# Kernel optimization log

Hardware: AMD Instinct MI355X
Metric: run time of the kernel (lower is better)

Reference implementation:

```python
import jax, jax.numpy as jnp
import numpy as np

N_NODES = 100000
N_EDGES = 1600000
N_FEAT = 128
HIDDEN = 128
N_CLASSES = 10
N_GRAPHS = 64


def setup_inputs() -> dict:
    key = jax.random.key(0)
    ks = jax.random.split(key, 9)
    x = jax.random.normal(ks[0], (N_NODES, N_FEAT), dtype=jnp.float32)
    edge_index = jax.random.randint(ks[1], (2, N_EDGES), 0, N_NODES, dtype=jnp.int64)
    batch = jnp.sort(jax.random.randint(ks[2], (N_NODES,), 0, N_GRAPHS, dtype=jnp.int64))
    # GCNConv weights (stored as [in, out] for x @ W) and biases
    s1 = 1.0 / np.sqrt(N_FEAT)
    s2 = 1.0 / np.sqrt(HIDDEN)
    W1 = jax.random.uniform(ks[3], (N_FEAT, HIDDEN), jnp.float32, -s1, s1)
    b1 = jnp.zeros((HIDDEN,), jnp.float32)
    W2 = jax.random.uniform(ks[4], (HIDDEN, HIDDEN), jnp.float32, -s2, s2)
    b2 = jnp.zeros((HIDDEN,), jnp.float32)
    Wfc = jax.random.uniform(ks[5], (HIDDEN, N_CLASSES), jnp.float32, -s2, s2)
    bfc = jax.random.uniform(ks[6], (N_CLASSES,), jnp.float32, -s2, s2)
    return {"x": x, "edge_index": edge_index, "batch": batch,
            "W1": W1, "b1": b1, "W2": W2, "b2": b2, "Wfc": Wfc, "bfc": bfc}


def gcn_conv(x, W, b, src, dst, n_nodes):
    # PyG GCNConv: add self-loops, symmetric normalization D^-1/2 A D^-1/2,
    # linear transform, scatter-add aggregation, plus bias.
    h = x @ W  # [N, H]
    deg = jax.ops.segment_sum(jnp.ones_like(dst, dtype=x.dtype), dst,
                              num_segments=n_nodes)  # in-degree incl. self loops
    dis = jnp.where(deg > 0, jax.lax.rsqrt(deg), 0.0)
    norm = dis[src] * dis[dst]  # [E+N]
    msg = h[src] * norm[:, None]  # gather + scale
    out = jax.ops.segment_sum(msg, dst, num_segments=n_nodes)  # scatter-add
    return out + b


def reference(x, edge_index, batch, W1, b1, W2, b2, Wfc, bfc):
    n = x.shape[0]
    loops = jnp.arange(n, dtype=edge_index.dtype)
    src = jnp.concatenate([edge_index[0], loops])
    dst = jnp.concatenate([edge_index[1], loops])

    h = jax.nn.relu(gcn_conv(x, W1, b1, src, dst, n))
    h = jax.nn.relu(gcn_conv(h, W2, b2, src, dst, n))

    # global_mean_pool over graph ids
    sums = jax.ops.segment_sum(h, batch, num_segments=N_GRAPHS)  # [B, H]
    cnts = jax.ops.segment_sum(jnp.ones((n,), h.dtype), batch,
                               num_segments=N_GRAPHS)
    pooled = sums / jnp.maximum(cnts, 1.0)[:, None]
    return pooled @ Wfc + bfc  # [B, C]
```

## Files before the change

kernel.cpp:

```cpp
#include <hip/hip_runtime.h>
#include <hip/hip_bf16.h>


typedef __attribute__((ext_vector_type(8))) short s16x8;
typedef __attribute__((ext_vector_type(4))) float f32x4;

#define BSH 9
#define BNODES 512
#define SRC_BITS 17
#define SRC_MASK ((1u << SRC_BITS) - 1u)
#define EPB 4096
#define NPART 8
#define PSH 14

__device__ inline float bflo(unsigned int u) { return __uint_as_float(u << 16); }
__device__ inline float bfhi(unsigned int u) { return __uint_as_float(u & 0xFFFF0000u); }
__device__ inline unsigned short f2bf(float f) {
    unsigned int u = __float_as_uint(f);
    unsigned int r = (u + 0x7FFFu + ((u >> 16) & 1u)) >> 16;
    return (unsigned short)r;
}
__device__ inline unsigned int packbf2(float a, float b) {
    return (unsigned int)f2bf(a) | ((unsigned int)f2bf(b) << 16);
}

__global__ __launch_bounds__(512) void bucket_scatter_kernel(const int* __restrict__ src, const int* __restrict__ dst,
                                                             int E, int cap, int* __restrict__ gfill,
                                                             unsigned int* __restrict__ gbuf, int nsc,
                                                             const float* __restrict__ W1, const float* __restrict__ W2,
                                                             short* __restrict__ WT1, short* __restrict__ WT2,
                                                             short* __restrict__ bufA, int n) {
    __shared__ int hist[256];
    __shared__ int loff[256];
    __shared__ int basea[256];
    __shared__ int rk[256];
    __shared__ int wsum[4];
    __shared__ unsigned int sorted[EPB];
    __shared__ unsigned char bko[EPB];
    int t = threadIdx.x;
    if ((int)blockIdx.x >= nsc) {
        int g = ((int)blockIdx.x - nsc) * 512 + t;
        const float* W = (g < 16384) ? W1 : W2;
        short* WT = (g < 16384) ? WT1 : WT2;
        int tt = g & 16383;
        int k = tt >> 7, nn = tt & 127;
        WT[nn * 128 + k] = f2bf(W[tt]);
        if ((int)blockIdx.x == nsc && t < 64) ((unsigned int*)(bufA + (size_t)n * 128))[t] = 0u;
        return;
    }
    if (t < 256) { hist[t] = 0; rk[t] = 0; }
    __syncthreads();
    int e0 = blockIdx.x * EPB;
    unsigned int wreg[EPB / 512];
    int breg[EPB / 512];
    #pragma unroll
    for (int i = 0; i < EPB / 512; i++) {
        int e = e0 + i * 512 + t;
        if (e < E) {
            int d = dst[e], s = src[e];
            int b = d >> BSH;
            wreg[i] = ((unsigned int)(d & (BNODES - 1)) << SRC_BITS) | (unsigned int)s;
            breg[i] = b;
            atomicAdd(&hist[b], 1);
        } else breg[i] = -1;
    }
    __syncthreads();
    int h = 0, incl = 0;
    if (t < 256) {
        h = hist[t];
        incl = h;
        int lane = t & 63;
        #pragma unroll
        for (int d = 1; d < 64; d <<= 1) {
            int u = __shfl_up(incl, d);
            if (lane >= d) incl += u;
        }
        if (lane == 63) wsum[t >> 6] = incl;
    }
    __syncthreads();
    if (t < 256) {
        int w = t >> 6;
        int wbase = 0;
        #pragma unroll
        for (int i = 0; i < 4; i++) if (i < w) wbase += wsum[i];
        loff[t] = wbase + incl - h;
        basea[t] = (h > 0) ? atomicAdd(&gfill[t], h) : 0;
    }
    __syncthreads();
    #pragma unroll
    for (int i = 0; i < EPB / 512; i++) {
        int b = breg[i];
        if (b >= 0) {
            int slot = loff[b] + atomicAdd(&rk[b], 1);
            sorted[slot] = wreg[i];
            bko[slot] = (unsigned char)b;
        }
    }
    __syncthreads();
    int ntot = loff[255] + hist[255];
    for (int i = t; i < ntot; i += 512) {
        int b = bko[i];
        int pos = basea[b] + (i - loff[b]);
        if (pos < cap) gbuf[(size_t)b * cap + pos] = sorted[i];
    }
}

__global__ __launch_bounds__(1024) void bucket_countfill_kernel(const unsigned int* __restrict__ gbuf,
                                                                const int* __restrict__ gfill, int cap, int n,
                                                                int* __restrict__ cnt, int* __restrict__ offA,
                                                                float* __restrict__ dis, int* __restrict__ g_total,
                                                                int* __restrict__ csr) {
    int b = blockIdx.x, t = threadIdx.x;
    int d0 = b << BSH;
    __shared__ int cl2[BNODES * NPART];
    __shared__ int nodeoff[BNODES];
    __shared__ int wsum[4];
    __shared__ int gbase_s;
    for (int i = t; i < BNODES * NPART; i += 1024) cl2[i] = 0;
    __syncthreads();
    int ne = min(gfill[b], cap);
    const unsigned int* eb = gbuf + (size_t)b * cap;
    for (int i = t; i < ne; i += 1024) {
        unsigned int wd = eb[i];
        int li = wd >> SRC_BITS;
        int part = (int)((wd & SRC_MASK) >> PSH);
        atomicAdd(&cl2[li * NPART + part], 1);
    }
    __syncthreads();
    int v0 = 0, v1 = 0, p0 = 0, p1 = 0, incl = 0, s = 0;
    if (t < 256) {
        #pragma unroll
        for (int j = 0; j < NPART; j++) v0 += cl2[(2 * t) * NPART + j];
        #pragma unroll
        for (int j = 0; j < NPART; j++) v1 += cl2[(2 * t + 1) * NPART + j];
        p0 = (v0 + 7) & ~7; p1 = (v1 + 7) & ~7;
        s = p0 + p1;
        incl = s;
        int lane = t & 63;
        #pragma unroll
        for (int dd = 1; dd < 64; dd <<= 1) {
            int u = __shfl_up(incl, dd);
            if (lane >= dd) incl += u;
        }
        if (lane == 63) wsum[t >> 6] = incl;
    }
    __syncthreads();
    if (t == 0) gbase_s = atomicAdd(g_total, wsum[0] + wsum[1] + wsum[2] + wsum[3]);
    __syncthreads();
    if (t < 256) {
        int w = t >> 6;
        int wbase = 0;
        #pragma unroll
        for (int i = 0; i < 4; i++) if (i < w) wbase += wsum[i];
        int excl = wbase + incl - s;
        int gbase = gbase_s;
        int o0 = gbase + excl, o1 = o0 + p0;
        int i0 = d0 + 2 * t, i1 = i0 + 1;
        if (i0 < n) { cnt[i0] = p0; offA[i0] = o0; dis[i0] = rsqrtf((float)(v0 + 1)); }
        if (i1 < n) { cnt[i1] = p1; offA[i1] = o1; dis[i1] = rsqrtf((float)(v1 + 1)); }
        nodeoff[2 * t] = o0; nodeoff[2 * t + 1] = o1;
    }
    __syncthreads();
    if (t < BNODES) {
        int run = nodeoff[t];
        #pragma unroll
        for (int j = 0; j < NPART; j++) {
            int c = cl2[t * NPART + j];
            cl2[t * NPART + j] = run;
            run += c;
        }
    }
    __syncthreads();
    for (int i = t; i < ne; i += 1024) {
        unsigned int wd = eb[i];
        int li = wd >> SRC_BITS;
        int part = (int)((wd & SRC_MASK) >> PSH);
        int slot = atomicAdd(&cl2[li * NPART + part], 1);
        csr[slot] = (int)(wd & SRC_MASK);
    }
    __syncthreads();
    if (t < BNODES) {
        int base = nodeoff[t];
        int end = cl2[t * NPART + NPART - 1];
        int p = ((end - base) + 7) & ~7;
        for (int j = end; j < base + p; j++) csr[j] = n;
    }
}

template <bool F32IN>
__global__ __launch_bounds__(256) void gemm_mfma_kernel(const void* __restrict__ Xv, const short* __restrict__ WTb,
                                                        const float* __restrict__ dis,
                                                        short* __restrict__ Yb, int n, int ntiles) {
    int lane = threadIdx.x & 63;
    int m = lane & 15, kg = lane >> 4;
    int gwave = (int)((blockIdx.x * 256 + threadIdx.x) >> 6);
    if (gwave >= ntiles) return;

    s16x8 bfr[8][4];
    #pragma unroll
    for (int t = 0; t < 8; t++)
        #pragma unroll
        for (int ks = 0; ks < 4; ks++)
            bfr[t][ks] = *(const s16x8*)(WTb + ((m * 8 + t) * 128 + ks * 32 + kg * 8));

    int rbase = gwave * 16;
    int row = rbase + m;
    size_t rc = (size_t)(row < n ? row : n - 1);
    s16x8 afr[4];
    if constexpr (F32IN) {
        const float* xrow = (const float*)Xv + rc * 128 + kg * 8;
        #pragma unroll
        for (int ks = 0; ks < 4; ks++) {
            float4 a0 = *(const float4*)(xrow + ks * 32);
            float4 a1 = *(const float4*)(xrow + ks * 32 + 4);
            s16x8 f;
            f[0] = (short)f2bf(a0.x); f[1] = (short)f2bf(a0.y);
            f[2] = (short)f2bf(a0.z); f[3] = (short)f2bf(a0.w);
            f[4] = (short)f2bf(a1.x); f[5] = (short)f2bf(a1.y);
            f[6] = (short)f2bf(a1.z); f[7] = (short)f2bf(a1.w);
            afr[ks] = f;
        }
    } else {
        const short* xrow = (const short*)Xv + rc * 128 + kg * 8;
        #pragma unroll
        for (int ks = 0; ks < 4; ks++) afr[ks] = *(const s16x8*)(xrow + ks * 32);
    }
    f32x4 acc[8];
    #pragma unroll
    for (int t = 0; t < 8; t++) acc[t] = (f32x4)(0.f);
    #pragma unroll
    for (int ks = 0; ks < 4; ks++)
        #pragma unroll
        for (int t = 0; t < 8; t++)
            acc[t] = __builtin_amdgcn_mfma_f32_16x16x32_bf16(afr[ks], bfr[t][ks], acc[t], 0, 0, 0);
    int orow0 = rbase + kg * 4;
    #pragma unroll
    for (int r = 0; r < 4; r++) {
        int orow = orow0 + r;
        if (orow < n) {
            float dv = dis[orow];
            s16x8 y;
            #pragma unroll
            for (int t = 0; t < 8; t++) y[t] = (short)f2bf(acc[t][r] * dv);
            *(s16x8*)(Yb + (size_t)orow * 128 + m * 8) = y;
        }
    }
}

__global__ __launch_bounds__(256) void agg_kernel(const short* __restrict__ H, const int* __restrict__ csr,
                                                  const int* __restrict__ offA, const int* __restrict__ cnt,
                                                  const float* __restrict__ dis, const float* __restrict__ bias,
                                                  short* __restrict__ O, int n) {
    int wid = __builtin_amdgcn_readfirstlane((int)((blockIdx.x * 256 + threadIdx.x) >> 6));
    int lane = threadIdx.x & 63;
    int half = lane >> 5, fl = lane & 31;
    if (wid >= n) return;
    int base = __builtin_amdgcn_readfirstlane(offA[wid]);
    int c = __builtin_amdgcn_readfirstlane(cnt[wid]);
    float d = dis[wid];
    float a0 = 0.f, a1 = 0.f, a2 = 0.f, a3 = 0.f;
    if (half == 0) {
        uint2 sv = ((const uint2*)(H + (size_t)wid * 128))[fl];
        a0 = bflo(sv.x); a1 = bfhi(sv.x);
        a2 = bflo(sv.y); a3 = bfhi(sv.y);
    }
    for (int k = 0; k < c; k += 8) {
        int4 q0 = *(const int4*)(csr + base + k);
        int4 q1 = *(const int4*)(csr + base + k + 4);
        int r0 = half ? q0.y : q0.x;
        int r1 = half ? q0.w : q0.z;
        int r2 = half ? q1.y : q1.x;
        int r3 = half ? q1.w : q1.z;
        uint2 h0 = ((const uint2*)(H + (size_t)r0 * 128))[fl];
        uint2 h1 = ((const uint2*)(H + (size_t)r1 * 128))[fl];
        uint2 h2 = ((const uint2*)(H + (size_t)r2 * 128))[fl];
        uint2 h3 = ((const uint2*)(H + (size_t)r3 * 128))[fl];
        a0 += bflo(h0.x); a1 += bfhi(h0.x); a2 += bflo(h0.y); a3 += bfhi(h0.y);
        a0 += bflo(h1.x); a1 += bfhi(h1.x); a2 += bflo(h1.y); a3 += bfhi(h1.y);
        a0 += bflo(h2.x); a1 += bfhi(h2.x); a2 += bflo(h2.y); a3 += bfhi(h2.y);
        a0 += bflo(h3.x); a1 += bfhi(h3.x); a2 += bflo(h3.y); a3 += bfhi(h3.y);
    }
    a0 += __shfl_xor(a0, 32);
    a1 += __shfl_xor(a1, 32);
    a2 += __shfl_xor(a2, 32);
    a3 += __shfl_xor(a3, 32);
    if (half == 0) {
        float4 b = ((const float4*)bias)[fl];
        float o0 = a0 * d + b.x, o1 = a1 * d + b.y;
        float o2 = a2 * d + b.z, o3 = a3 * d + b.w;
        o0 = fmaxf(o0, 0.f); o1 = fmaxf(o1, 0.f);
        o2 = fmaxf(o2, 0.f); o3 = fmaxf(o3, 0.f);
        ((uint2*)(O + (size_t)wid * 128))[fl] = make_uint2(packbf2(o0, o1), packbf2(o2, o3));
    }
}

__global__ __launch_bounds__(1024) void poolfc_kernel(const short* __restrict__ H, const int* __restrict__ batch,
                                                      const float* __restrict__ Wfc, const float* __restrict__ bfc,
                                                      float* __restrict__ out, int n) {
    int g = blockIdx.x;
    int t = threadIdx.x;
    int w = t >> 6, lane = t & 63;
    int q = lane >> 4, fl4 = lane & 15;
    int lo = 0, hi = n;
    while (lo < hi) { int mid = (lo + hi) >> 1; if (batch[mid] < g) lo = mid + 1; else hi = mid; }
    int lo2 = lo; hi = n;
    while (lo2 < hi) { int mid = (lo2 + hi) >> 1; if (batch[mid] < g + 1) lo2 = mid + 1; else hi = mid; }
    float ac[8];
    #pragma unroll
    for (int j = 0; j < 8; j++) ac[j] = 0.f;
    for (int i = lo + w * 4 + q; i < lo2; i += 64) {
        uint4 u = ((const uint4*)(H + (size_t)i * 128))[fl4];
        ac[0] += bflo(u.x); ac[1] += bfhi(u.x);
        ac[2] += bflo(u.y); ac[3] += bfhi(u.y);
        ac[4] += bflo(u.z); ac[5] += bfhi(u.z);
        ac[6] += bflo(u.w); ac[7] += bfhi(u.w);
    }
    #pragma unroll
    for (int j = 0; j < 8; j++) {
        ac[j] += __shfl_xor(ac[j], 16);
        ac[j] += __shfl_xor(ac[j], 32);
    }
    __shared__ float red[16][128];
    if (lane < 16) {
        #pragma unroll
        for (int j = 0; j < 8; j++) red[w][fl4 * 8 + j] = ac[j];
    }
    __syncthreads();
    __shared__ float pv[128];
    if (w == 0) {
        float s0 = 0.f, s1 = 0.f;
        #pragma unroll
        for (int r = 0; r < 16; r++) { s0 += red[r][2 * lane]; s1 += red[r][2 * lane + 1]; }
        float inv = 1.0f / fmaxf((float)(lo2 - lo), 1.0f);
        pv[2 * lane] = s0 * inv;
        pv[2 * lane + 1] = s1 * inv;
    }
    __syncthreads();
    if (t < 10) {
        float acc = 0.f;
        for (int k = 0; k < 128; k++) acc += pv[k] * Wfc[k * 10 + t];
        out[g * 10 + t] = acc + bfc[t];
    }
}

extern "C" void kernel_launch(void* const* d_in, const int* in_sizes, int n_in,
                              void* d_out, int out_size, void* d_ws, size_t ws_size,
                              hipStream_t stream) {
    const float* x   = (const float*)d_in[0];
    const int*   ei  = (const int*)d_in[1];
    const int*   bat = (const int*)d_in[2];
    const float* W1  = (const float*)d_in[3];
    const float* b1  = (const float*)d_in[4];
    const float* W2  = (const float*)d_in[5];
    const float* b2  = (const float*)d_in[6];
    const float* Wfc = (const float*)d_in[7];
    const float* bfc = (const float*)d_in[8];
    int n = in_sizes[0] / 128;
    int E = in_sizes[1] / 2;
    const int* src = ei;
    const int* dst = ei + E;

    int nbuck = (n + BNODES - 1) >> BSH;
    int cap = ((E / nbuck) * 2 + 512 + 63) & ~63;

    char* ws = (char*)d_ws;
    size_t off = 0;
    auto alloc = [&](size_t bytes) -> void* {
        void* p = ws + off;
        off = (off + bytes + 511) & ~(size_t)511;
        return p;
    };
    int*   gfill  = (int*)alloc(256 * 4);
    int*   gtotal = (int*)alloc(512);
    size_t zero_bytes = off;
    int*   cnt   = (int*)alloc((size_t)n * 4);
    int*   offA  = (int*)alloc((size_t)n * 4);
    float* dis   = (float*)alloc((size_t)n * 4);
    unsigned int* gbuf = (unsigned int*)alloc((size_t)nbuck * cap * 4);
    int*   csr   = (int*)alloc(((size_t)E + 8 * (size_t)(n + 1)) * 4);
    short* wt1   = (short*)alloc(128 * 128 * 2);
    short* wt2   = (short*)alloc(128 * 128 * 2);
    short* bufA  = (short*)alloc((size_t)(n + 1) * 128 * 2);
    short* bufB  = (short*)alloc((size_t)(n + 1) * 128 * 2);
    (void)ws_size;

    int ntiles = (n + 15) / 16;
    int gemm_blocks = (ntiles + 3) / 4;
    int nsc = (E + EPB - 1) / EPB;

    hipMemsetAsync(d_ws, 0, zero_bytes, stream);
    bucket_scatter_kernel<<<nsc + 64, 512, 0, stream>>>(src, dst, E, cap, gfill, gbuf, nsc,
                                                        W1, W2, wt1, wt2, bufA, n);
    bucket_countfill_kernel<<<nbuck, 1024, 0, stream>>>(gbuf, gfill, cap, n, cnt, offA, dis, gtotal, csr);

    gemm_mfma_kernel<true><<<gemm_blocks, 256, 0, stream>>>(x, wt1, dis, bufA, n, ntiles);
    agg_kernel<<<((size_t)n * 64 + 255) / 256, 256, 0, stream>>>(bufA, csr, offA, cnt, dis, b1, bufB, n);
    gemm_mfma_kernel<false><<<gemm_blocks, 256, 0, stream>>>(bufB, wt2, dis, bufA, n, ntiles);
    agg_kernel<<<((size_t)n * 64 + 255) / 256, 256, 0, stream>>>(bufA, csr, offA, cnt, dis, b2, bufB, n);

    poolfc_kernel<<<64, 1024, 0, stream>>>(bufB, bat, Wfc, bfc, (float*)d_out, n);
}
```

Measured before the change: 332.8 us.

## Fuse CSR build with first GEMM, stage weights in LDS, split pooling

Buckets now hold 256 nodes and the CSR build drops its per-source partitioning, so rows are padded to 4 instead of 8. The first-layer GEMM runs in the same launch as the CSR build, as extra blocks that no longer need dis, so it can proceed without waiting for degrees. The source-side normalization moves into the first aggregation, which now gathers dis per neighbour. Both GEMMs stage the transposed weights in LDS across 1024-thread blocks instead of loading them into registers per wave. Pooling is split into a 256-block partial-sum kernel and a small FC kernel to raise parallelism. The cost is extra gathers of dis in layer-1 aggregation, plus a changed sort locality that drops the source partitioning.

```diff
diff --git a/kernel.cpp b/kernel.cpp
--- a/kernel.cpp
+++ b/kernel.cpp
@@ -5,13 +5,11 @@
 typedef __attribute__((ext_vector_type(8))) short s16x8;
 typedef __attribute__((ext_vector_type(4))) float f32x4;
 
-#define BSH 9
-#define BNODES 512
+#define BSH 8
+#define BNODES 256
 #define SRC_BITS 17
 #define SRC_MASK ((1u << SRC_BITS) - 1u)
 #define EPB 4096
-#define NPART 8
-#define PSH 14
 
 __device__ inline float bflo(unsigned int u) { return __uint_as_float(u << 16); }
 __device__ inline float bfhi(unsigned int u) { return __uint_as_float(u & 0xFFFF0000u); }
@@ -30,13 +28,13 @@
                                                              const float* __restrict__ W1, const float* __restrict__ W2,
                                                              short* __restrict__ WT1, short* __restrict__ WT2,
                                                              short* __restrict__ bufA, int n) {
-    __shared__ int hist[256];
-    __shared__ int loff[256];
-    __shared__ int basea[256];
-    __shared__ int rk[256];
-    __shared__ int wsum[4];
+    __shared__ int hist[512];
+    __shared__ int loff[512];
+    __shared__ int basea[512];
+    __shared__ int rk[512];
+    __shared__ int wsum[8];
     __shared__ unsigned int sorted[EPB];
-    __shared__ unsigned char bko[EPB];
+    __shared__ unsigned short bko[EPB];
     int t = threadIdx.x;
     if ((int)blockIdx.x >= nsc) {
         int g = ((int)blockIdx.x - nsc) * 512 + t;
@@ -48,7 +46,7 @@
         if ((int)blockIdx.x == nsc && t < 64) ((unsigned int*)(bufA + (size_t)n * 128))[t] = 0u;
         return;
     }
-    if (t < 256) { hist[t] = 0; rk[t] = 0; }
+    hist[t] = 0; rk[t] = 0;
     __syncthreads();
     int e0 = blockIdx.x * EPB;
     unsigned int wreg[EPB / 512];
@@ -65,10 +63,9 @@
         } else breg[i] = -1;
     }
     __syncthreads();
-    int h = 0, incl = 0;
-    if (t < 256) {
-        h = hist[t];
-        incl = h;
+    int h = hist[t];
+    int incl = h;
+    {
         int lane = t & 63;
         #pragma unroll
         for (int d = 1; d < 64; d <<= 1) {
@@ -78,11 +75,11 @@
         if (lane == 63) wsum[t >> 6] = incl;
     }
     __syncthreads();
-    if (t < 256) {
+    {
         int w = t >> 6;
         int wbase = 0;
         #pragma unroll
-        for (int i = 0; i < 4; i++) if (i < w) wbase += wsum[i];
+        for (int i = 0; i < 8; i++) if (i < w) wbase += wsum[i];
         loff[t] = wbase + incl - h;
         basea[t] = (h > 0) ? atomicAdd(&gfill[t], h) : 0;
     }
@@ -93,11 +90,11 @@
         if (b >= 0) {
             int slot = loff[b] + atomicAdd(&rk[b], 1);
             sorted[slot] = wreg[i];
-            bko[slot] = (unsigned char)b;
-        }
-    }
-    __syncthreads();
-    int ntot = loff[255] + hist[255];
+            bko[slot] = (unsigned short)b;
+        }
+    }
+    __syncthreads();
+    int ntot = loff[511] + hist[511];
     for (int i = t; i < ntot; i += 512) {
         int b = bko[i];
         int pos = basea[b] + (i - loff[b]);
@@ -105,105 +102,23 @@
     }
 }
 
-__global__ __launch_bounds__(1024) void bucket_countfill_kernel(const unsigned int* __restrict__ gbuf,
-                                                                const int* __restrict__ gfill, int cap, int n,
-                                                                int* __restrict__ cnt, int* __restrict__ offA,
-                                                                float* __restrict__ dis, int* __restrict__ g_total,
-                                                                int* __restrict__ csr) {
-    int b = blockIdx.x, t = threadIdx.x;
-    int d0 = b << BSH;
-    __shared__ int cl2[BNODES * NPART];
-    __shared__ int nodeoff[BNODES];
-    __shared__ int wsum[4];
-    __shared__ int gbase_s;
-    for (int i = t; i < BNODES * NPART; i += 1024) cl2[i] = 0;
-    __syncthreads();
-    int ne = min(gfill[b], cap);
-    const unsigned int* eb = gbuf + (size_t)b * cap;
-    for (int i = t; i < ne; i += 1024) {
-        unsigned int wd = eb[i];
-        int li = wd >> SRC_BITS;
-        int part = (int)((wd & SRC_MASK) >> PSH);
-        atomicAdd(&cl2[li * NPART + part], 1);
-    }
-    __syncthreads();
-    int v0 = 0, v1 = 0, p0 = 0, p1 = 0, incl = 0, s = 0;
-    if (t < 256) {
-        #pragma unroll
-        for (int j = 0; j < NPART; j++) v0 += cl2[(2 * t) * NPART + j];
-        #pragma unroll
-        for (int j = 0; j < NPART; j++) v1 += cl2[(2 * t + 1) * NPART + j];
-        p0 = (v0 + 7) & ~7; p1 = (v1 + 7) & ~7;
-        s = p0 + p1;
-        incl = s;
-        int lane = t & 63;
-        #pragma unroll
-        for (int dd = 1; dd < 64; dd <<= 1) {
-            int u = __shfl_up(incl, dd);
-            if (lane >= dd) incl += u;
-        }
-        if (lane == 63) wsum[t >> 6] = incl;
-    }
-    __syncthreads();
-    if (t == 0) gbase_s = atomicAdd(g_total, wsum[0] + wsum[1] + wsum[2] + wsum[3]);
-    __syncthreads();
-    if (t < 256) {
-        int w = t >> 6;
-        int wbase = 0;
-        #pragma unroll
-        for (int i = 0; i < 4; i++) if (i < w) wbase += wsum[i];
-        int excl = wbase + incl - s;
-        int gbase = gbase_s;
-        int o0 = gbase + excl, o1 = o0 + p0;
-        int i0 = d0 + 2 * t, i1 = i0 + 1;
-        if (i0 < n) { cnt[i0] = p0; offA[i0] = o0; dis[i0] = rsqrtf((float)(v0 + 1)); }
-        if (i1 < n) { cnt[i1] = p1; offA[i1] = o1; dis[i1] = rsqrtf((float)(v1 + 1)); }
-        nodeoff[2 * t] = o0; nodeoff[2 * t + 1] = o1;
-    }
-    __syncthreads();
-    if (t < BNODES) {
-        int run = nodeoff[t];
-        #pragma unroll
-        for (int j = 0; j < NPART; j++) {
-            int c = cl2[t * NPART + j];
-            cl2[t * NPART + j] = run;
-            run += c;
-        }
-    }
-    __syncthreads();
-    for (int i = t; i < ne; i += 1024) {
-        unsigned int wd = eb[i];
-        int li = wd >> SRC_BITS;
-        int part = (int)((wd & SRC_MASK) >> PSH);
-        int slot = atomicAdd(&cl2[li * NPART + part], 1);
-        csr[slot] = (int)(wd & SRC_MASK);
-    }
-    __syncthreads();
-    if (t < BNODES) {
-        int base = nodeoff[t];
-        int end = cl2[t * NPART + NPART - 1];
-        int p = ((end - base) + 7) & ~7;
-        for (int j = end; j < base + p; j++) csr[j] = n;
-    }
-}
-
-template <bool F32IN>
-__global__ __launch_bounds__(256) void gemm_mfma_kernel(const void* __restrict__ Xv, const short* __restrict__ WTb,
-                                                        const float* __restrict__ dis,
-                                                        short* __restrict__ Yb, int n, int ntiles) {
-    int lane = threadIdx.x & 63;
+__device__ __forceinline__ void stage_w(short* wl, const short* __restrict__ WTb, int t, int nthreads) {
+    for (int s = t; s < 2048; s += nthreads) {
+        int tt = s >> 8, ks = (s >> 6) & 3, ln = s & 63;
+        int m = ln & 15, kg = ln >> 4;
+        *(s16x8*)(wl + s * 8) = *(const s16x8*)(WTb + ((m * 8 + tt) * 128 + ks * 32 + kg * 8));
+    }
+}
+
+template <bool F32IN, bool SCALED>
+__device__ __forceinline__ void gemm_body(const void* __restrict__ Xv, const short* wl,
+                                          const float* __restrict__ dis, short* __restrict__ Yb,
+                                          int n, int ntiles, int tile_base, int t) {
+    int wid = t >> 6, lane = t & 63;
     int m = lane & 15, kg = lane >> 4;
-    int gwave = (int)((blockIdx.x * 256 + threadIdx.x) >> 6);
-    if (gwave >= ntiles) return;
-
-    s16x8 bfr[8][4];
-    #pragma unroll
-    for (int t = 0; t < 8; t++)
-        #pragma unroll
-        for (int ks = 0; ks < 4; ks++)
-            bfr[t][ks] = *(const s16x8*)(WTb + ((m * 8 + t) * 128 + ks * 32 + kg * 8));
-
-    int rbase = gwave * 16;
+    int gw = tile_base + wid;
+    if (gw >= ntiles) return;
+    int rbase = gw * 16;
     int row = rbase + m;
     size_t rc = (size_t)(row < n ? row : n - 1);
     s16x8 afr[4];
@@ -227,26 +142,110 @@
     }
     f32x4 acc[8];
     #pragma unroll
-    for (int t = 0; t < 8; t++) acc[t] = (f32x4)(0.f);
-    #pragma unroll
-    for (int ks = 0; ks < 4; ks++)
-        #pragma unroll
-        for (int t = 0; t < 8; t++)
-            acc[t] = __builtin_amdgcn_mfma_f32_16x16x32_bf16(afr[ks], bfr[t][ks], acc[t], 0, 0, 0);
+    for (int i = 0; i < 8; i++) acc[i] = (f32x4)(0.f);
+    #pragma unroll
+    for (int ks = 0; ks < 4; ks++) {
+        s16x8 bfr[8];
+        #pragma unroll
+        for (int t8 = 0; t8 < 8; t8++)
+            bfr[t8] = *(const s16x8*)(wl + ((t8 * 4 + ks) * 64 + lane) * 8);
+        #pragma unroll
+        for (int t8 = 0; t8 < 8; t8++)
+            acc[t8] = __builtin_amdgcn_mfma_f32_16x16x32_bf16(afr[ks], bfr[t8], acc[t8], 0, 0, 0);
+    }
     int orow0 = rbase + kg * 4;
     #pragma unroll
     for (int r = 0; r < 4; r++) {
         int orow = orow0 + r;
         if (orow < n) {
-            float dv = dis[orow];
+            float dv = SCALED ? dis[orow] : 1.0f;
             s16x8 y;
             #pragma unroll
-            for (int t = 0; t < 8; t++) y[t] = (short)f2bf(acc[t][r] * dv);
+            for (int t8 = 0; t8 < 8; t8++) y[t8] = (short)f2bf(acc[t8][r] * dv);
             *(s16x8*)(Yb + (size_t)orow * 128 + m * 8) = y;
         }
     }
 }
 
+__global__ __launch_bounds__(1024) void build_gemm_kernel(const unsigned int* __restrict__ gbuf,
+                                                          const int* __restrict__ gfill, int cap, int n, int nbuck,
+                                                          int* __restrict__ cnt, int* __restrict__ offA,
+                                                          float* __restrict__ dis, int* __restrict__ g_total,
+                                                          int* __restrict__ csr,
+                                                          const float* __restrict__ X, const short* __restrict__ WTb,
+                                                          short* __restrict__ Yb, int ntiles) {
+    __shared__ short wlds[2048 * 8];
+    __shared__ int cl[BNODES];
+    __shared__ int wsum[4];
+    __shared__ int gbase_s;
+    int t = threadIdx.x;
+    int bid = blockIdx.x;
+    if (bid >= nbuck) {
+        stage_w(wlds, WTb, t, 1024);
+        __syncthreads();
+        gemm_body<true, false>(X, wlds, nullptr, Yb, n, ntiles, (bid - nbuck) * 16, t);
+        return;
+    }
+    int d0 = bid << BSH;
+    if (t < BNODES) cl[t] = 0;
+    if (bid == 0 && t == 256) dis[n] = 0.f;
+    __syncthreads();
+    int ne = min(gfill[bid], cap);
+    const unsigned int* eb = gbuf + (size_t)bid * cap;
+    for (int i = t; i < ne; i += 1024) atomicAdd(&cl[eb[i] >> SRC_BITS], 1);
+    __syncthreads();
+    int v = 0, p = 0, o = 0;
+    if (t < BNODES) {
+        v = cl[t];
+        p = (v + 3) & ~3;
+        int incl = p;
+        int lane = t & 63;
+        #pragma unroll
+        for (int dd = 1; dd < 64; dd <<= 1) {
+            int u = __shfl_up(incl, dd);
+            if (lane >= dd) incl += u;
+        }
+        if (lane == 63) wsum[t >> 6] = incl;
+        cl[t] = incl - p;
+    }
+    __syncthreads();
+    if (t == 0) gbase_s = atomicAdd(g_total, wsum[0] + wsum[1] + wsum[2] + wsum[3]);
+    __syncthreads();
+    if (t < BNODES) {
+        int w = t >> 6;
+        int wbase = 0;
+        #pragma unroll
+        for (int i = 0; i < 4; i++) if (i < w) wbase += wsum[i];
+        o = gbase_s + wbase + cl[t];
+        int node = d0 + t;
+        if (node < n) { cnt[node] = p; offA[node] = o; dis[node] = rsqrtf((float)(v + 1)); }
+    }
+    __syncthreads();
+    if (t < BNODES) cl[t] = o;
+    __syncthreads();
+    for (int i = t; i < ne; i += 1024) {
+        unsigned int wd = eb[i];
+        int li = wd >> SRC_BITS;
+        int slot = atomicAdd(&cl[li], 1);
+        csr[slot] = (int)(wd & SRC_MASK);
+    }
+    __syncthreads();
+    if (t < BNODES) {
+        for (int j = o + v; j < o + p; j++) csr[j] = n;
+    }
+}
+
+__global__ __launch_bounds__(1024) void gemm_lds_kernel(const short* __restrict__ Xb, const short* __restrict__ WTb,
+                                                        const float* __restrict__ dis, short* __restrict__ Yb,
+                                                        int n, int ntiles) {
+    __shared__ short wlds[2048 * 8];
+    int t = threadIdx.x;
+    stage_w(wlds, WTb, t, 1024);
+    __syncthreads();
+    gemm_body<false, true>(Xb, wlds, dis, Yb, n, ntiles, blockIdx.x * 16, t);
+}
+
+template <bool SCALE_SRC>
 __global__ __launch_bounds__(256) void agg_kernel(const short* __restrict__ H, const int* __restrict__ csr,
                                                   const int* __restrict__ offA, const int* __restrict__ cnt,
                                                   const float* __restrict__ dis, const float* __restrict__ bias,
@@ -261,10 +260,12 @@
     float a0 = 0.f, a1 = 0.f, a2 = 0.f, a3 = 0.f;
     if (half == 0) {
         uint2 sv = ((const uint2*)(H + (size_t)wid * 128))[fl];
-        a0 = bflo(sv.x); a1 = bfhi(sv.x);
-        a2 = bflo(sv.y); a3 = bfhi(sv.y);
-    }
-    for (int k = 0; k < c; k += 8) {
+        float sc = SCALE_SRC ? d : 1.0f;
+        a0 = sc * bflo(sv.x); a1 = sc * bfhi(sv.x);
+        a2 = sc * bflo(sv.y); a3 = sc * bfhi(sv.y);
+    }
+    int k = 0;
+    for (; k + 8 <= c; k += 8) {
         int4 q0 = *(const int4*)(csr + base + k);
         int4 q1 = *(const int4*)(csr + base + k + 4);
         int r0 = half ? q0.y : q0.x;
@@ -275,10 +276,33 @@
         uint2 h1 = ((const uint2*)(H + (size_t)r1 * 128))[fl];
         uint2 h2 = ((const uint2*)(H + (size_t)r2 * 128))[fl];
         uint2 h3 = ((const uint2*)(H + (size_t)r3 * 128))[fl];
-        a0 += bflo(h0.x); a1 += bfhi(h0.x); a2 += bflo(h0.y); a3 += bfhi(h0.y);
-        a0 += bflo(h1.x); a1 += bfhi(h1.x); a2 += bflo(h1.y); a3 += bfhi(h1.y);
-        a0 += bflo(h2.x); a1 += bfhi(h2.x); a2 += bflo(h2.y); a3 += bfhi(h2.y);
-        a0 += bflo(h3.x); a1 += bfhi(h3.x); a2 += bflo(h3.y); a3 += bfhi(h3.y);
+        if constexpr (SCALE_SRC) {
+            float w0 = dis[r0], w1 = dis[r1], w2 = dis[r2], w3 = dis[r3];
+            a0 += w0 * bflo(h0.x); a1 += w0 * bfhi(h0.x); a2 += w0 * bflo(h0.y); a3 += w0 * bfhi(h0.y);
+            a0 += w1 * bflo(h1.x); a1 += w1 * bfhi(h1.x); a2 += w1 * bflo(h1.y); a3 += w1 * bfhi(h1.y);
+            a0 += w2 * bflo(h2.x); a1 += w2 * bfhi(h2.x); a2 += w2 * bflo(h2.y); a3 += w2 * bfhi(h2.y);
+            a0 += w3 * bflo(h3.x); a1 += w3 * bfhi(h3.x); a2 += w3 * bflo(h3.y); a3 += w3 * bfhi(h3.y);
+        } else {
+            a0 += bflo(h0.x); a1 += bfhi(h0.x); a2 += bflo(h0.y); a3 += bfhi(h0.y);
+            a0 += bflo(h1.x); a1 += bfhi(h1.x); a2 += bflo(h1.y); a3 += bfhi(h1.y);
+            a0 += bflo(h2.x); a1 += bfhi(h2.x); a2 += bflo(h2.y); a3 += bfhi(h2.y);
+            a0 += bflo(h3.x); a1 += bfhi(h3.x); a2 += bflo(h3.y); a3 += bfhi(h3.y);
+        }
+    }
+    if (k < c) {
+        int4 q = *(const int4*)(csr + base + k);
+        int r0 = half ? q.y : q.x;
+        int r1 = half ? q.w : q.z;
+        uint2 h0 = ((const uint2*)(H + (size_t)r0 * 128))[fl];
+        uint2 h1 = ((const uint2*)(H + (size_t)r1 * 128))[fl];
+        if constexpr (SCALE_SRC) {
+            float w0 = dis[r0], w1 = dis[r1];
+            a0 += w0 * bflo(h0.x); a1 += w0 * bfhi(h0.x); a2 += w0 * bflo(h0.y); a3 += w0 * bfhi(h0.y);
+            a0 += w1 * bflo(h1.x); a1 += w1 * bfhi(h1.x); a2 += w1 * bflo(h1.y); a3 += w1 * bfhi(h1.y);
+        } else {
+            a0 += bflo(h0.x); a1 += bfhi(h0.x); a2 += bflo(h0.y); a3 += bfhi(h0.y);
+            a0 += bflo(h1.x); a1 += bfhi(h1.x); a2 += bflo(h1.y); a3 += bfhi(h1.y);
+        }
     }
     a0 += __shfl_xor(a0, 32);
     a1 += __shfl_xor(a1, 32);
@@ -294,21 +318,24 @@
     }
 }
 
-__global__ __launch_bounds__(1024) void poolfc_kernel(const short* __restrict__ H, const int* __restrict__ batch,
-                                                      const float* __restrict__ Wfc, const float* __restrict__ bfc,
-                                                      float* __restrict__ out, int n) {
-    int g = blockIdx.x;
+__global__ __launch_bounds__(256) void poolA_kernel(const short* __restrict__ H, const int* __restrict__ batch,
+                                                    float* __restrict__ part, int* __restrict__ cntg, int n) {
+    int bid = blockIdx.x;
+    int g = bid >> 2, q = bid & 3;
     int t = threadIdx.x;
     int w = t >> 6, lane = t & 63;
-    int q = lane >> 4, fl4 = lane & 15;
+    int qq = lane >> 4, fl4 = lane & 15;
     int lo = 0, hi = n;
     while (lo < hi) { int mid = (lo + hi) >> 1; if (batch[mid] < g) lo = mid + 1; else hi = mid; }
     int lo2 = lo; hi = n;
     while (lo2 < hi) { int mid = (lo2 + hi) >> 1; if (batch[mid] < g + 1) lo2 = mid + 1; else hi = mid; }
+    int len = lo2 - lo;
+    int qlo = lo + (len * q) / 4;
+    int qhi = lo + (len * (q + 1)) / 4;
     float ac[8];
     #pragma unroll
     for (int j = 0; j < 8; j++) ac[j] = 0.f;
-    for (int i = lo + w * 4 + q; i < lo2; i += 64) {
+    for (int i = qlo + w * 4 + qq; i < qhi; i += 16) {
         uint4 u = ((const uint4*)(H + (size_t)i * 128))[fl4];
         ac[0] += bflo(u.x); ac[1] += bfhi(u.x);
         ac[2] += bflo(u.y); ac[3] += bfhi(u.y);
@@ -320,21 +347,31 @@
         ac[j] += __shfl_xor(ac[j], 16);
         ac[j] += __shfl_xor(ac[j], 32);
     }
-    __shared__ float red[16][128];
+    __shared__ float red[4][128];
     if (lane < 16) {
         #pragma unroll
         for (int j = 0; j < 8; j++) red[w][fl4 * 8 + j] = ac[j];
     }
     __syncthreads();
+    if (t < 128) part[(size_t)bid * 128 + t] = red[0][t] + red[1][t] + red[2][t] + red[3][t];
+    if (q == 0 && t == 0) cntg[g] = len;
+}
+
+__global__ __launch_bounds__(64) void poolB_kernel(const float* __restrict__ part, const int* __restrict__ cntg,
+                                                   const float* __restrict__ Wfc, const float* __restrict__ bfc,
+                                                   float* __restrict__ out) {
+    int g = blockIdx.x;
+    int t = threadIdx.x;
     __shared__ float pv[128];
-    if (w == 0) {
-        float s0 = 0.f, s1 = 0.f;
-        #pragma unroll
-        for (int r = 0; r < 16; r++) { s0 += red[r][2 * lane]; s1 += red[r][2 * lane + 1]; }
-        float inv = 1.0f / fmaxf((float)(lo2 - lo), 1.0f);
-        pv[2 * lane] = s0 * inv;
-        pv[2 * lane + 1] = s1 * inv;
-    }
+    float inv = 1.0f / fmaxf((float)cntg[g], 1.0f);
+    float s0 = 0.f, s1 = 0.f;
+    #pragma unroll
+    for (int q = 0; q < 4; q++) {
+        s0 += part[(size_t)(g * 4 + q) * 128 + 2 * t];
+        s1 += part[(size_t)(g * 4 + q) * 128 + 2 * t + 1];
+    }
+    pv[2 * t] = s0 * inv;
+    pv[2 * t + 1] = s1 * inv;
     __syncthreads();
     if (t < 10) {
         float acc = 0.f;
@@ -370,33 +407,35 @@
         off = (off + bytes + 511) & ~(size_t)511;
         return p;
     };
-    int*   gfill  = (int*)alloc(256 * 4);
+    int*   gfill  = (int*)alloc(512 * 4);
     int*   gtotal = (int*)alloc(512);
     size_t zero_bytes = off;
     int*   cnt   = (int*)alloc((size_t)n * 4);
     int*   offA  = (int*)alloc((size_t)n * 4);
-    float* dis   = (float*)alloc((size_t)n * 4);
+    float* dis   = (float*)alloc((size_t)(n + 1) * 4);
     unsigned int* gbuf = (unsigned int*)alloc((size_t)nbuck * cap * 4);
-    int*   csr   = (int*)alloc(((size_t)E + 8 * (size_t)(n + 1)) * 4);
+    int*   csr   = (int*)alloc(((size_t)E + 4 * (size_t)(n + 1)) * 4);
     short* wt1   = (short*)alloc(128 * 128 * 2);
     short* wt2   = (short*)alloc(128 * 128 * 2);
     short* bufA  = (short*)alloc((size_t)(n + 1) * 128 * 2);
     short* bufB  = (short*)alloc((size_t)(n + 1) * 128 * 2);
+    float* part  = (float*)alloc(256 * 128 * 4);
+    int*   cntg  = (int*)alloc(64 * 4);
     (void)ws_size;
 
     int ntiles = (n + 15) / 16;
-    int gemm_blocks = (ntiles + 3) / 4;
+    int gemm_blocks = (ntiles + 15) / 16;
     int nsc = (E + EPB - 1) / EPB;
 
     hipMemsetAsync(d_ws, 0, zero_bytes, stream);
     bucket_scatter_kernel<<<nsc + 64, 512, 0, stream>>>(src, dst, E, cap, gfill, gbuf, nsc,
                                                         W1, W2, wt1, wt2, bufA, n);
-    bucket_countfill_kernel<<<nbuck, 1024, 0, stream>>>(gbuf, gfill, cap, n, cnt, offA, dis, gtotal, csr);
-
-    gemm_mfma_kernel<true><<<gemm_blocks, 256, 0, stream>>>(x, wt1, dis, bufA, n, ntiles);
-    agg_kernel<<<((size_t)n * 64 + 255) / 256, 256, 0, stream>>>(bufA, csr, offA, cnt, dis, b1, bufB, n);
-    gemm_mfma_kernel<false><<<gemm_blocks, 256, 0, stream>>>(bufB, wt2, dis, bufA, n, ntiles);
-    agg_kernel<<<((size_t)n * 64 + 255) / 256, 256, 0, stream>>>(bufA, csr, offA, cnt, dis, b2, bufB, n);
-
-    poolfc_kernel<<<64, 1024, 0, stream>>>(bufB, bat, Wfc, bfc, (float*)d_out, n);
-}
+    build_gemm_kernel<<<nbuck + gemm_blocks, 1024, 0, stream>>>(gbuf, gfill, cap, n, nbuck,
+                                                                cnt, offA, dis, gtotal, csr,
+                                                                x, wt1, bufA, ntiles);
+    agg_kernel<true><<<((size_t)n * 64 + 255) / 256, 256, 0, stream>>>(bufA, csr, offA, cnt, dis, b1, bufB, n);
+    gemm_lds_kernel<<<gemm_blocks, 1024, 0, stream>>>(bufB, wt2, dis, bufA, n, ntiles);
+    agg_kernel<false><<<((size_t)n * 64 + 255) / 256, 256, 0, stream>>>(bufA, csr, offA, cnt, dis, b2, bufB, n);
+    poolA_kernel<<<256, 256, 0, stream>>>(bufB, bat, part, cntg, n);
+    poolB_kernel<<<64, 64, 0, stream>>>(part, cntg, Wfc, bfc, (float*)d_out);
+}
```

After: 290.6 us. 1.15x faster.
